# Kernel tuning notes

Hardware: AMD Instinct MI355X
Metric: run time of the kernel (lower is better)

Reference implementation:

```python
import jax, jax.numpy as jnp
import numpy as np

K = 3       # kernel_size
STRIDE = 1
PAD = 1
EPS = 1e-12  # F.normalize eps


def setup_inputs() -> dict:
    key = jax.random.key(0)
    k1, k2, k3 = jax.random.split(key, 3)
    x = jax.random.normal(k1, (8, 128, 112, 112), dtype=jnp.float32)
    weight = jax.random.normal(k2, (256, 128, K, K), dtype=jnp.float32)
    bias = jax.random.normal(k3, (256,), dtype=jnp.float32)
    return {"x": x, "weight": weight, "bias": bias}


def reference(x, weight, bias):
    B, C, H, W = x.shape
    Cout = weight.shape[0]
    oh = (H + 2 * PAD - K) // STRIDE + 1
    ow = (W + 2 * PAD - K) // STRIDE + 1
    # im2col: [B, C*K*K, oh, ow]; feature order (C, kh, kw), same as torch F.unfold
    patches = jax.lax.conv_general_dilated_patches(
        x, (K, K), (STRIDE, STRIDE), [(PAD, PAD), (PAD, PAD)],
        dimension_numbers=("NCHW", "OIHW", "NCHW"))
    u = patches.reshape(B, C * K * K, oh * ow)
    # L2-normalize each patch column (dim=1), matching F.normalize(p=2, dim=1)
    norm = jnp.sqrt(jnp.sum(u * u, axis=1, keepdims=True))
    u = u / jnp.maximum(norm, EPS)
    # GEMM: [Cout, C*K*K] x [B, C*K*K, L] -> [B, Cout, L]
    out = jnp.einsum("od,bdl->bol", weight.reshape(Cout, -1), u)
    out = out.reshape(B, Cout, oh, ow) + bias[None, :, None, None]
    return out
```

## Files before the change

kernel.cpp:

```cpp
#include <hip/hip_runtime.h>

#define CIN    128
#define COUT   256
#define Hh     112
#define Ww     112
#define HW     12544
#define NBATCH 8
#define NPIX   (NBATCH*HW)
#define KD     (CIN*9)
#define PH     114
#define PPIX   (NBATCH*PH*PH)

typedef __bf16         v8bf __attribute__((ext_vector_type(8)));
typedef float          v4f  __attribute__((ext_vector_type(4)));

__device__ __forceinline__ unsigned short f2bf(float f) {
  unsigned int u = __float_as_uint(f);
  u += 0x7FFFu + ((u >> 16) & 1u);
  return (unsigned short)(u >> 16);
}

__device__ __forceinline__ void gl_lds16(const void* g, void* l) {
  __builtin_amdgcn_global_load_lds(
      (const __attribute__((address_space(1))) void*)g,
      (__attribute__((address_space(3))) void*)l, 16, 0, 0);
}

#define SQS 65
__global__ __launch_bounds__(256) void k_sq_convert(
    const float* __restrict__ x, unsigned short* __restrict__ xbp,
    float* __restrict__ sq)
{
  __shared__ unsigned int US[56 * SQS];
  __shared__ float sqp[56 * 4];

  int tid = threadIdx.x;
  int l   = tid & 63;
  int wid = tid >> 6;
  int bid = blockIdx.x;
  int xh  = bid & 1;
  int t2  = bid >> 1;
  int b   = t2 / Hh;
  int oy  = t2 - b * Hh;
  int ox0 = xh * 56;

  const float* xp = x + (size_t)b * CIN * HW + oy * Ww + ox0;
  bool valid = l < 56;
  float acc = 0.0f;
#pragma unroll
  for (int it = 0; it < 16; ++it) {
    int cp = it * 4 + wid;
    int c0 = cp * 2;
    float v0 = 0.0f, v1 = 0.0f;
    if (valid) {
      v0 = xp[(size_t)c0 * HW + l];
      v1 = xp[(size_t)(c0 + 1) * HW + l];
    }
    acc += v0 * v0 + v1 * v1;
    unsigned int pk = (unsigned int)f2bf(v0) | ((unsigned int)f2bf(v1) << 16);
    if (valid) US[l * SQS + cp] = pk;
  }
  if (valid) sqp[l * 4 + wid] = acc;
  __syncthreads();

  if (tid < 56) {
    float s = sqp[tid * 4] + sqp[tid * 4 + 1] + sqp[tid * 4 + 2] + sqp[tid * 4 + 3];
    sq[(size_t)b * HW + oy * Ww + ox0 + tid] = s;
  }

  unsigned int* dst = (unsigned int*)xbp +
      ((size_t)(b * PH + oy + 1) * PH + (ox0 + 1)) * (CIN / 2);
  for (int h = tid; h < 896; h += 256) {
    int u0  = h * 4;
    int pix = u0 >> 6, cu = u0 & 63;
    const unsigned int* s = &US[pix * SQS + cu];
    uint4 vv; vv.x = s[0]; vv.y = s[1]; vv.z = s[2]; vv.w = s[3];
    *(uint4*)(dst + u0) = vv;
  }
}

__global__ __launch_bounds__(256) void k_zero_border(unsigned short* __restrict__ xbp)
{
  int gid = blockIdx.x * 256 + threadIdx.x;
  if (gid >= PPIX) return;
  int b  = gid / (PH * PH);
  int r  = gid - b * PH * PH;
  int py = r / PH;
  int px = r - py * PH;
  if (py != 0 && py != PH - 1 && px != 0 && px != PH - 1) return;
  unsigned int* dst = (unsigned int*)xbp + (size_t)gid * (CIN / 2);
  uint4 z = {0, 0, 0, 0};
#pragma unroll
  for (int c0 = 0; c0 < 64; c0 += 4) *(uint4*)(dst + c0) = z;
}

__global__ __launch_bounds__(256) void k_invnorm(
    const float* __restrict__ sq, float* __restrict__ invn)
{
  int p = blockIdx.x * 256 + threadIdx.x;
  if (p >= NPIX) return;
  int b  = p / HW;  int r  = p - b * HW;
  int oy = r / Ww;  int ox = r - oy * Ww;
  const float* s = sq + (size_t)b * HW;
  float acc = 0.0f;
#pragma unroll
  for (int dy = -1; dy <= 1; ++dy) {
    int iy = oy + dy;
    if (iy < 0 || iy >= Hh) continue;
#pragma unroll
    for (int dx = -1; dx <= 1; ++dx) {
      int ix = ox + dx;
      if (ix < 0 || ix >= Ww) continue;
      acc += s[iy * Ww + ix];
    }
  }
  invn[p] = 1.0f / fmaxf(sqrtf(acc), 1e-12f);
}

__global__ __launch_bounds__(256) void k_packw(
    const float* __restrict__ w, unsigned short* __restrict__ wp)
{
  int idx = blockIdx.x * 256 + threadIdx.x;
  int o  = idx / KD;
  int rr = idx - o * KD;
  int kk = rr >> 7;
  int c  = rr & 127;
  wp[idx] = f2bf(w[(size_t)o * KD + c * 9 + kk]);
}

#define SLAB_S 132
__global__ __launch_bounds__(256, 3) void k_conv(
    const unsigned short* __restrict__ wp,
    const unsigned short* __restrict__ xbp,
    const float* __restrict__ invn,
    const float* __restrict__ bias,
    float* __restrict__ out)
{
  __shared__ __align__(16) char smem[64 * SLAB_S * 4];
  unsigned short* As = (unsigned short*)smem;
  unsigned short* Bs = As + 128 * 64;
  float* slab = (float*)smem;

  int tid  = threadIdx.x;
  int lane = tid & 63;
  int wid  = tid >> 6;
  int wm   = wid >> 1, wn = wid & 1;
  int quad = lane >> 4;
  int l16  = lane & 15;

  int L  = blockIdx.x;
  int g  = L >> 4;
  int j  = L & 15;
  int bn = g * 8 + (j & 7);
  int bm = j >> 3;

  int srow = tid >> 3;
  int g16  = (tid & 7) ^ (srow & 7);

  const unsigned short* asrc = wp + (size_t)(bm * 128 + srow) * KD + g16 * 8;

  int pb[4];
#pragma unroll
  for (int jj = 0; jj < 4; ++jj) {
    int n  = bn * 128 + jj * 32 + srow;
    int b  = n / HW;  int r  = n - b * HW;
    int oy = r / Ww;  int ox = r - oy * Ww;
    pb[jj] = ((b * PH + oy) * PH + ox) * CIN + g16 * 8;
  }

  v4f acc[4][4];
#pragma unroll
  for (int mt = 0; mt < 4; ++mt)
#pragma unroll
    for (int nt = 0; nt < 4; ++nt)
#pragma unroll
      for (int q = 0; q < 4; ++q) acc[mt][nt][q] = 0.0f;

  const int khs[9] = {0,0,0,1,1,1,2,2,2};
  const int kws[9] = {0,1,2,0,1,2,0,1,2};

  for (int s = 0; s < 18; ++s) {
    int kk   = s >> 1;
    int c0   = (s & 1) * 64;
    int soff = (khs[kk] * PH + kws[kk]) * CIN + c0;

#pragma unroll
    for (int jj = 0; jj < 4; ++jj)
      gl_lds16(asrc + (size_t)jj * 32 * KD + s * 64,
               &As[(wid * 8 + jj * 32) * 64]);
#pragma unroll
    for (int jj = 0; jj < 4; ++jj)
      gl_lds16(xbp + pb[jj] + soff,
               &Bs[(wid * 8 + jj * 32) * 64]);

    __syncthreads();

#pragma unroll
    for (int h = 0; h < 2; ++h) {
      v8bf af[4], bf[4];
      int cch = (h * 4 + quad) ^ (l16 & 7);
#pragma unroll
      for (int mt = 0; mt < 4; ++mt)
        af[mt] = *(const v8bf*)&As[(wm * 64 + mt * 16 + l16) * 64 + cch * 8];
#pragma unroll
      for (int nt = 0; nt < 4; ++nt)
        bf[nt] = *(const v8bf*)&Bs[(wn * 64 + nt * 16 + l16) * 64 + cch * 8];
#pragma unroll
      for (int mt = 0; mt < 4; ++mt)
#pragma unroll
        for (int nt = 0; nt < 4; ++nt)
          acc[mt][nt] = __builtin_amdgcn_mfma_f32_16x16x32_bf16(
              af[mt], bf[nt], acc[mt][nt], 0, 0, 0);
    }

    __syncthreads();
  }

  int nbase = bn * 128;
  int bb = nbase / HW;
  int rr = nbase - bb * HW;
  float* obase = out + (size_t)bb * COUT * HW + rr;

  float invv[4];
#pragma unroll
  for (int nt = 0; nt < 4; ++nt)
    invv[nt] = invn[nbase + wn * 64 + nt * 16 + l16];

  for (int pass = 0; pass < 2; ++pass) {
    if (pass) __syncthreads();
    if (wm == pass) {
#pragma unroll
      for (int mt = 0; mt < 4; ++mt)
#pragma unroll
        for (int nt = 0; nt < 4; ++nt) {
          int col = wn * 64 + nt * 16 + l16;
#pragma unroll
          for (int reg = 0; reg < 4; ++reg)
            slab[(mt * 16 + quad * 4 + reg) * SLAB_S + col] =
                acc[mt][nt][reg] * invv[nt];
        }
    }
    __syncthreads();
#pragma unroll
    for (int it = 0; it < 2; ++it) {
      int row = it * 32 + (tid >> 3);
      int o   = bm * 128 + pass * 64 + row;
      float bv = bias[o];
      float* orow = obase + (size_t)o * HW;
#pragma unroll
      for (int k = 0; k < 4; ++k) {
        int c4 = ((tid & 7) + k * 8) * 4;
        v4f v = *(const v4f*)&slab[row * SLAB_S + c4];
        v4f r2;
#pragma unroll
        for (int q = 0; q < 4; ++q) r2[q] = v[q] + bv;
        *(v4f*)(orow + c4) = r2;
      }
    }
  }
}

extern "C" void kernel_launch(void* const* d_in, const int* in_sizes, int n_in,
                              void* d_out, int out_size, void* d_ws, size_t ws_size,
                              hipStream_t stream) {
  const float* x    = (const float*)d_in[0];
  const float* w    = (const float*)d_in[1];
  const float* bias = (const float*)d_in[2];
  float* out        = (float*)d_out;

  char* ws = (char*)d_ws;
  unsigned short* xbp = (unsigned short*)ws;
  size_t off = (size_t)PPIX * CIN * 2;
  unsigned short* wpk = (unsigned short*)(ws + off);
  off += (size_t)COUT * KD * 2;
  float* sq = (float*)(ws + off);
  off += (size_t)NPIX * 4;
  float* invn = (float*)(ws + off);

  k_sq_convert<<<NBATCH * Hh * 2, 256, 0, stream>>>(x, xbp, sq);
  k_zero_border<<<(PPIX + 255) / 256, 256, 0, stream>>>(xbp);
  k_packw<<<(COUT * KD) / 256, 256, 0, stream>>>(w, wpk);
  k_invnorm<<<NPIX / 256, 256, 0, stream>>>(sq, invn);
  k_conv<<<1568, 256, 0, stream>>>(wpk, xbp, invn, bias, out);
}
```

Baseline: 211.4 us.

## Fuse preprocessing kernels and compute inverse norms inside conv kernel

Merges the input convert/square-sum, border zeroing and weight packing into a single preprocessing launch in which each block handles a full padded row, with the weight packing done by extra blocks. The 3x3 neighborhood sum for the inverse norm moves into the conv kernel prologue, which removes the separate invnorm kernel and its buffer. The conv kernel's occupancy hint rises from 3 to 4 blocks per CU. This cuts launch count and intermediate traffic, at the cost of redundant neighborhood reads in the conv prologue and possible register pressure under the tighter launch bound.

```diff
diff --git a/kernel.cpp b/kernel.cpp
--- a/kernel.cpp
+++ b/kernel.cpp
@@ -26,113 +26,99 @@
       (__attribute__((address_space(3))) void*)l, 16, 0, 0);
 }
 
-#define SQS 65
-__global__ __launch_bounds__(256) void k_sq_convert(
-    const float* __restrict__ x, unsigned short* __restrict__ xbp,
+#define USS 130
+__global__ __launch_bounds__(256) void k_pre(
+    const float* __restrict__ x, const float* __restrict__ w,
+    unsigned short* __restrict__ xbp, unsigned short* __restrict__ wpk,
     float* __restrict__ sq)
 {
-  __shared__ unsigned int US[56 * SQS];
-  __shared__ float sqp[56 * 4];
+  __shared__ unsigned short US[112 * USS];
+  __shared__ float sqp[112 * 4];
 
   int tid = threadIdx.x;
+  int bid = blockIdx.x;
+
+  if (bid >= NBATCH * PH) {
+    int t = (bid - NBATCH * PH) * 2048 + tid * 8;
+#pragma unroll
+    for (int i = 0; i < 8; ++i) {
+      int idx = t + i;
+      int o  = idx / KD;
+      int rr = idx - o * KD;
+      int kk = rr >> 7;
+      int c  = rr & 127;
+      wpk[idx] = f2bf(w[(size_t)o * KD + c * 9 + kk]);
+    }
+    return;
+  }
+
+  int b  = bid / PH;
+  int py = bid - b * PH;
+  unsigned int* dstrow = (unsigned int*)xbp +
+      (size_t)(b * PH + py) * PH * (CIN / 2);
+
+  if (py == 0 || py == PH - 1) {
+    uint4 z = {0, 0, 0, 0};
+    for (int h = tid; h < PH * (CIN / 8); h += 256)
+      *(uint4*)(dstrow + h * 4) = z;
+    return;
+  }
+
+  int oy  = py - 1;
   int l   = tid & 63;
   int wid = tid >> 6;
-  int bid = blockIdx.x;
-  int xh  = bid & 1;
-  int t2  = bid >> 1;
-  int b   = t2 / Hh;
-  int oy  = t2 - b * Hh;
-  int ox0 = xh * 56;
-
-  const float* xp = x + (size_t)b * CIN * HW + oy * Ww + ox0;
+  const float* xp = x + (size_t)b * CIN * HW + (size_t)oy * Ww;
   bool valid = l < 56;
-  float acc = 0.0f;
-#pragma unroll
-  for (int it = 0; it < 16; ++it) {
-    int cp = it * 4 + wid;
-    int c0 = cp * 2;
-    float v0 = 0.0f, v1 = 0.0f;
+
+  float a0 = 0.0f, a1 = 0.0f;
+#pragma unroll
+  for (int it = 0; it < 32; ++it) {
+    int c = wid * 32 + it;
+    float vx = 0.0f, vy = 0.0f;
     if (valid) {
-      v0 = xp[(size_t)c0 * HW + l];
-      v1 = xp[(size_t)(c0 + 1) * HW + l];
-    }
-    acc += v0 * v0 + v1 * v1;
-    unsigned int pk = (unsigned int)f2bf(v0) | ((unsigned int)f2bf(v1) << 16);
-    if (valid) US[l * SQS + cp] = pk;
-  }
-  if (valid) sqp[l * 4 + wid] = acc;
+      float2 v = *(const float2*)(xp + (size_t)c * HW + 2 * l);
+      vx = v.x; vy = v.y;
+    }
+    a0 += vx * vx;
+    a1 += vy * vy;
+    if (valid) {
+      US[(2 * l) * USS + c]     = f2bf(vx);
+      US[(2 * l + 1) * USS + c] = f2bf(vy);
+    }
+  }
+  if (valid) { sqp[(2 * l) * 4 + wid] = a0; sqp[(2 * l + 1) * 4 + wid] = a1; }
   __syncthreads();
 
-  if (tid < 56) {
+  if (tid < 112) {
     float s = sqp[tid * 4] + sqp[tid * 4 + 1] + sqp[tid * 4 + 2] + sqp[tid * 4 + 3];
-    sq[(size_t)b * HW + oy * Ww + ox0 + tid] = s;
-  }
-
-  unsigned int* dst = (unsigned int*)xbp +
-      ((size_t)(b * PH + oy + 1) * PH + (ox0 + 1)) * (CIN / 2);
-  for (int h = tid; h < 896; h += 256) {
-    int u0  = h * 4;
-    int pix = u0 >> 6, cu = u0 & 63;
-    const unsigned int* s = &US[pix * SQS + cu];
-    uint4 vv; vv.x = s[0]; vv.y = s[1]; vv.z = s[2]; vv.w = s[3];
-    *(uint4*)(dst + u0) = vv;
-  }
-}
-
-__global__ __launch_bounds__(256) void k_zero_border(unsigned short* __restrict__ xbp)
-{
-  int gid = blockIdx.x * 256 + threadIdx.x;
-  if (gid >= PPIX) return;
-  int b  = gid / (PH * PH);
-  int r  = gid - b * PH * PH;
-  int py = r / PH;
-  int px = r - py * PH;
-  if (py != 0 && py != PH - 1 && px != 0 && px != PH - 1) return;
-  unsigned int* dst = (unsigned int*)xbp + (size_t)gid * (CIN / 2);
-  uint4 z = {0, 0, 0, 0};
-#pragma unroll
-  for (int c0 = 0; c0 < 64; c0 += 4) *(uint4*)(dst + c0) = z;
-}
-
-__global__ __launch_bounds__(256) void k_invnorm(
-    const float* __restrict__ sq, float* __restrict__ invn)
-{
-  int p = blockIdx.x * 256 + threadIdx.x;
-  if (p >= NPIX) return;
-  int b  = p / HW;  int r  = p - b * HW;
-  int oy = r / Ww;  int ox = r - oy * Ww;
-  const float* s = sq + (size_t)b * HW;
-  float acc = 0.0f;
-#pragma unroll
-  for (int dy = -1; dy <= 1; ++dy) {
-    int iy = oy + dy;
-    if (iy < 0 || iy >= Hh) continue;
-#pragma unroll
-    for (int dx = -1; dx <= 1; ++dx) {
-      int ix = ox + dx;
-      if (ix < 0 || ix >= Ww) continue;
-      acc += s[iy * Ww + ix];
-    }
-  }
-  invn[p] = 1.0f / fmaxf(sqrtf(acc), 1e-12f);
-}
-
-__global__ __launch_bounds__(256) void k_packw(
-    const float* __restrict__ w, unsigned short* __restrict__ wp)
-{
-  int idx = blockIdx.x * 256 + threadIdx.x;
-  int o  = idx / KD;
-  int rr = idx - o * KD;
-  int kk = rr >> 7;
-  int c  = rr & 127;
-  wp[idx] = f2bf(w[(size_t)o * KD + c * 9 + kk]);
+    sq[(size_t)b * HW + (size_t)oy * Ww + tid] = s;
+  }
+
+  unsigned int* dst = dstrow + (CIN / 2);
+  for (int h = tid; h < 112 * 16; h += 256) {
+    int px = h >> 4, part = h & 15;
+    const unsigned short* s = &US[px * USS + part * 8];
+    uint4 vv;
+    vv.x = *(const unsigned int*)(s + 0);
+    vv.y = *(const unsigned int*)(s + 2);
+    vv.z = *(const unsigned int*)(s + 4);
+    vv.w = *(const unsigned int*)(s + 6);
+    *(uint4*)(dst + h * 4) = vv;
+  }
+
+  if (tid < 32) {
+    uint4 z = {0, 0, 0, 0};
+    int px   = (tid >> 4) ? (PH - 1) : 0;
+    int part = tid & 15;
+    *(uint4*)(dstrow + px * (CIN / 2) + part * 4) = z;
+  }
 }
 
 #define SLAB_S 132
-__global__ __launch_bounds__(256, 3) void k_conv(
+__global__ __launch_bounds__(256, 4) void k_conv(
     const unsigned short* __restrict__ wp,
     const unsigned short* __restrict__ xbp,
-    const float* __restrict__ invn,
+    const float* __restrict__ sq,
     const float* __restrict__ bias,
     float* __restrict__ out)
 {
@@ -168,6 +154,30 @@
     pb[jj] = ((b * PH + oy) * PH + ox) * CIN + g16 * 8;
   }
 
+  int nbase = bn * 128;
+
+  float invv[4];
+#pragma unroll
+  for (int nt = 0; nt < 4; ++nt) {
+    int n  = nbase + wn * 64 + nt * 16 + l16;
+    int b  = n / HW;  int r  = n - b * HW;
+    int oy = r / Ww;  int ox = r - oy * Ww;
+    const float* s = sq + (size_t)b * HW;
+    float acc = 0.0f;
+#pragma unroll
+    for (int dy = -1; dy <= 1; ++dy) {
+      int iy = oy + dy;
+      if (iy < 0 || iy >= Hh) continue;
+#pragma unroll
+      for (int dx = -1; dx <= 1; ++dx) {
+        int ix = ox + dx;
+        if (ix < 0 || ix >= Ww) continue;
+        acc += s[iy * Ww + ix];
+      }
+    }
+    invv[nt] = 1.0f / fmaxf(sqrtf(acc), 1e-12f);
+  }
+
   v4f acc[4][4];
 #pragma unroll
   for (int mt = 0; mt < 4; ++mt)
@@ -216,15 +226,9 @@
     __syncthreads();
   }
 
-  int nbase = bn * 128;
   int bb = nbase / HW;
   int rr = nbase - bb * HW;
   float* obase = out + (size_t)bb * COUT * HW + rr;
-
-  float invv[4];
-#pragma unroll
-  for (int nt = 0; nt < 4; ++nt)
-    invv[nt] = invn[nbase + wn * 64 + nt * 16 + l16];
 
   for (int pass = 0; pass < 2; ++pass) {
     if (pass) __syncthreads();
@@ -274,12 +278,7 @@
   unsigned short* wpk = (unsigned short*)(ws + off);
   off += (size_t)COUT * KD * 2;
   float* sq = (float*)(ws + off);
-  off += (size_t)NPIX * 4;
-  float* invn = (float*)(ws + off);
-
-  k_sq_convert<<<NBATCH * Hh * 2, 256, 0, stream>>>(x, xbp, sq);
-  k_zero_border<<<(PPIX + 255) / 256, 256, 0, stream>>>(xbp);
-  k_packw<<<(COUT * KD) / 256, 256, 0, stream>>>(w, wpk);
-  k_invnorm<<<NPIX / 256, 256, 0, stream>>>(sq, invn);
-  k_conv<<<1568, 256, 0, stream>>>(wpk, xbp, invn, bias, out);
-}
+
+  k_pre<<<NBATCH * PH + (COUT * KD) / 2048, 256, 0, stream>>>(x, w, xbp, wpk, sq);
+  k_conv<<<1568, 256, 0, stream>>>(wpk, xbp, sq, bias, out);
+}
```

New measurement: 206.0 us. 2.6% less time.
